# Kernel optimization log

Measured on AMD Instinct MI355X. Metric: run time of the kernel, lower is better.

Reference implementation:

```python
import jax, jax.numpy as jnp
import numpy as np

N_NODES = 50000
N_RAND_EDGES = 500000
SELF_LOOP_W = 0.5  # fill_value in add_remaining_self_loops


def _build_graph(key):
    k1, k2, k3 = jax.random.split(key, 3)
    src = jax.random.randint(k1, (N_RAND_EDGES,), 0, N_NODES)
    dst = jax.random.randint(k2, (N_RAND_EDGES,), 0, N_NODES)
    # PPMI weights are positive log-ratios; simulate with positive uniforms
    w = jax.random.uniform(k3, (N_RAND_EDGES,), minval=0.1, maxval=2.0)
    loops = jnp.arange(N_NODES)
    row = jnp.concatenate([src, loops])
    col = jnp.concatenate([dst, loops])
    ew = jnp.concatenate([w, jnp.full((N_NODES,), SELF_LOOP_W, dtype=w.dtype)])
    # symmetric normalization: D^-1/2 A D^-1/2 (deg computed from row, as in norm())
    deg = jax.ops.segment_sum(ew, row, num_segments=N_NODES)
    dis = jnp.where(deg > 0, deg ** -0.5, 0.0)
    norm = (dis[row] * ew * dis[col]).astype(jnp.float32)
    edge_index = jnp.stack([row, col]).astype(jnp.int64)
    return edge_index, norm


def setup_inputs() -> dict:
    key = jax.random.key(0)
    kx, kg, kw1, kw2 = jax.random.split(key, 4)
    edge_index, norm = _build_graph(kg)
    feat, hid, emb = 256, 128, 64
    # glorot init
    s1 = np.sqrt(6.0 / (feat + hid))
    s2 = np.sqrt(6.0 / (hid + emb))
    return {
        "x": jax.random.normal(kx, (N_NODES, feat), dtype=jnp.float32),
        "edge_index": edge_index,
        "norm": norm,
        "W1": jax.random.uniform(kw1, (feat, hid), minval=-s1, maxval=s1, dtype=jnp.float32),
        "b1": jnp.zeros((hid,), dtype=jnp.float32),
        "W2": jax.random.uniform(kw2, (hid, emb), minval=-s2, maxval=s2, dtype=jnp.float32),
        "b2": jnp.zeros((emb,), dtype=jnp.float32),
    }


def _gcn_layer(x, row, col, norm, W, b):
    h = x @ W                                   # [N, out]
    msg = norm[:, None] * h[row]                # gather + scale per edge
    agg = jax.ops.segment_sum(msg, col, num_segments=N_NODES)  # scatter-add
    return agg + b


def reference(x, edge_index, norm, W1, b1, W2, b2):
    row, col = edge_index[0], edge_index[1]
    h = _gcn_layer(x, row, col, norm, W1, b1)
    h = jax.nn.relu(h)  # dropout is identity in eval
    return _gcn_layer(h, row, col, norm, W2, b2)
```

## Files before the change

### kernel.cpp

```cpp
#include <hip/hip_runtime.h>
#include <stdint.h>


typedef __attribute__((ext_vector_type(8))) short short8;
typedef __attribute__((ext_vector_type(4))) float f32x4;

#define SLOTS 48
#define OCAP  65536

__device__ __forceinline__ unsigned short f2bf(float f) {
    unsigned u = __float_as_uint(f);
    return (unsigned short)((u + 0x7FFFu + ((u >> 16) & 1u)) >> 16);
}
__device__ __forceinline__ float bf_lo(unsigned v) { return __uint_as_float(v << 16); }
__device__ __forceinline__ float bf_hi(unsigned v) { return __uint_as_float(v & 0xFFFF0000u); }
__device__ __forceinline__ float bf1(unsigned short v) { return __uint_as_float((unsigned)v << 16); }
__device__ __forceinline__ unsigned short f2h(float f) {
    _Float16 h = (_Float16)f;
    return __builtin_bit_cast(unsigned short, h);
}
__device__ __forceinline__ float h2f(unsigned u16) {
    _Float16 h = __builtin_bit_cast(_Float16, (unsigned short)(u16 & 0xFFFFu));
    return (float)h;
}

__global__ __launch_bounds__(256) void k_prep(unsigned* __restrict__ ent, int entWords,
                                              int* __restrict__ cursor, int n,
                                              int* __restrict__ ocount,
                                              const int* __restrict__ ei,
                                              const float* __restrict__ nrm,
                                              int E, int N,
                                              unsigned* __restrict__ rec,
                                              const float* __restrict__ W1,
                                              const float* __restrict__ W2,
                                              unsigned short* __restrict__ W1t,
                                              unsigned short* __restrict__ W2t,
                                              int FEAT, int HID, int EMB) {
    __shared__ int sIs64;
    if (threadIdx.x < 64) {
        const int i = 1 + 2 * threadIdx.x;
        int z = (i < 2 * E) ? (ei[i] == 0) : 1;
        unsigned long long m = __ballot(z);
        if (threadIdx.x == 0) sIs64 = (m == ~0ULL) ? 1 : 0;
    }
    __syncthreads();
    const int is64 = sIs64;

    const int gid = blockIdx.x * blockDim.x + threadIdx.x;
    const int stride = gridDim.x * blockDim.x;
    if (gid == 0) *ocount = 0;

    int4* e4 = (int4*)ent;
    for (int j = gid; j < entWords / 4; j += stride) e4[j] = make_int4(0, 0, 0, 0);
    int4* c4 = (int4*)cursor;
    const int n4 = n >> 2;
    for (int j = gid; j < n4; j += stride) c4[j] = make_int4(0, 0, 0, 0);
    for (int j = (n4 << 2) + gid; j < n; j += stride) cursor[j] = 0;

    const int t1 = FEAT * HID, t2 = HID * EMB;
    for (int i = gid; i < t1 + t2; i += stride) {
        if (i < t1) {
            int k = i / HID, nn = i % HID;
            W1t[(size_t)nn * FEAT + k] = f2bf(W1[i]);
        } else {
            int j = i - t1;
            int k = j / EMB, nn = j % EMB;
            W2t[(size_t)nn * HID + k] = f2bf(W2[j]);
        }
    }

    const int nG = (E + 3) / 4;
    for (int g = gid; g < nG; g += stride) {
        const int e0 = g * 4;
        if (e0 + 3 < E) {
            int r[4], c[4];
            if (is64) {
                const int4* pr = (const int4*)(ei + 2 * e0);
                const int4* pc = (const int4*)(ei + 2 * E + 2 * e0);
                int4 r01 = pr[0], r23 = pr[1], c01 = pc[0], c23 = pc[1];
                r[0] = r01.x; r[1] = r01.z; r[2] = r23.x; r[3] = r23.z;
                c[0] = c01.x; c[1] = c01.z; c[2] = c23.x; c[3] = c23.z;
            } else {
                int4 rr = *(const int4*)(ei + e0);
                int4 cc = *(const int4*)(ei + E + e0);
                r[0] = rr.x; r[1] = rr.y; r[2] = rr.z; r[3] = rr.w;
                c[0] = cc.x; c[1] = cc.y; c[2] = cc.z; c[3] = cc.w;
            }
            const float4 w4 = *(const float4*)(nrm + e0);
            const float wv[4] = {w4.x, w4.y, w4.z, w4.w};
            unsigned ow[8];
            #pragma unroll
            for (int i = 0; i < 4; ++i) {
                unsigned a = 0xFFFFFFFFu, b = 0u;
                if ((unsigned)c[i] < (unsigned)N && (unsigned)r[i] < (unsigned)N) {
                    a = ((unsigned)r[i] << 16) | (unsigned)c[i];
                    b = (unsigned)f2h(wv[i]);
                }
                ow[2 * i + 0] = a;
                ow[2 * i + 1] = b;
            }
            uint4* dst = (uint4*)(rec + 2 * (size_t)e0);
            dst[0] = make_uint4(ow[0], ow[1], ow[2], ow[3]);
            dst[1] = make_uint4(ow[4], ow[5], ow[6], ow[7]);
        } else {
            for (int i = 0; i < 4; ++i) {
                const int e = e0 + i;
                unsigned a = 0xFFFFFFFFu, b = 0u;
                if (e < E) {
                    int rr, cc;
                    if (is64) { rr = ei[2 * e]; cc = ei[2 * (E + e)]; }
                    else      { rr = ei[e];     cc = ei[E + e]; }
                    if ((unsigned)cc < (unsigned)N && (unsigned)rr < (unsigned)N) {
                        a = ((unsigned)rr << 16) | (unsigned)cc;
                        b = (unsigned)f2h(nrm[e]);
                    }
                }
                rec[2 * (size_t)e + 0] = a;
                rec[2 * (size_t)e + 1] = b;
            }
        }
    }
}

template <int BM, int BN, int FM, int FN, bool A_F32, bool OUT_BF16>
__device__ __forceinline__ void gemm_body(char* ldsA, char* ldsB,
                                          const void* __restrict__ Ag,
                                          const unsigned short* __restrict__ Bt,
                                          void* __restrict__ Cv,
                                          int M, int K, int N, int blk) {
    const int tid  = threadIdx.x;
    const int lane = tid & 63;
    const int wid  = tid >> 6;
    const int wr   = wid >> 1;
    const int wc   = wid & 1;
    const int m0   = blk * BM;

    f32x4 acc[FM][FN] = {};

    for (int k0 = 0; k0 < K; k0 += 64) {
        {
            const int row  = tid >> 2;
            const int kq   = tid & 3;
            const int grow = min(m0 + row, M - 1);
            const int kbb  = kq * 32;
            const int sw   = (row & 7) << 4;
            if (A_F32) {
                const float* src = (const float*)Ag + (size_t)grow * K + k0 + kq * 16;
                float4 v0 = ((const float4*)src)[0];
                float4 v1 = ((const float4*)src)[1];
                float4 v2 = ((const float4*)src)[2];
                float4 v3 = ((const float4*)src)[3];
                union { short8 s; unsigned short h[8]; } p0, p1;
                p0.h[0] = f2bf(v0.x); p0.h[1] = f2bf(v0.y);
                p0.h[2] = f2bf(v0.z); p0.h[3] = f2bf(v0.w);
                p0.h[4] = f2bf(v1.x); p0.h[5] = f2bf(v1.y);
                p0.h[6] = f2bf(v1.z); p0.h[7] = f2bf(v1.w);
                p1.h[0] = f2bf(v2.x); p1.h[1] = f2bf(v2.y);
                p1.h[2] = f2bf(v2.z); p1.h[3] = f2bf(v2.w);
                p1.h[4] = f2bf(v3.x); p1.h[5] = f2bf(v3.y);
                p1.h[6] = f2bf(v3.z); p1.h[7] = f2bf(v3.w);
                *(short8*)(ldsA + row * 128 + ( kbb       ^ sw)) = p0.s;
                *(short8*)(ldsA + row * 128 + ((kbb + 16) ^ sw)) = p1.s;
            } else {
                const unsigned short* src =
                    (const unsigned short*)Ag + (size_t)grow * K + k0 + kq * 16;
                short8 s0 = ((const short8*)src)[0];
                short8 s1 = ((const short8*)src)[1];
                *(short8*)(ldsA + row * 128 + ( kbb       ^ sw)) = s0;
                *(short8*)(ldsA + row * 128 + ((kbb + 16) ^ sw)) = s1;
            }
        }
        if (BN == 128 || tid < 128) {
            const int row = tid >> 1;
            const int kh  = tid & 1;
            const int sw  = (row & 7) << 4;
            const short8* src = (const short8*)(Bt + (size_t)row * K + k0 + kh * 32);
            #pragma unroll
            for (int j = 0; j < 4; ++j) {
                short8 s = src[j];
                int kb = kh * 64 + j * 16;
                *(short8*)(ldsB + row * 128 + (kb ^ sw)) = s;
            }
        }
        __syncthreads();

        #pragma unroll
        for (int s = 0; s < 2; ++s) {
            const int klo = s * 64 + (lane >> 4) * 16;
            short8 af[FM], bfv[FN];
            #pragma unroll
            for (int i = 0; i < FM; ++i) {
                int r = wr * (FM * 16) + i * 16 + (lane & 15);
                af[i] = *(const short8*)(ldsA + r * 128 + (klo ^ ((r & 7) << 4)));
            }
            #pragma unroll
            for (int j = 0; j < FN; ++j) {
                int n = wc * (FN * 16) + j * 16 + (lane & 15);
                bfv[j] = *(const short8*)(ldsB + n * 128 + (klo ^ ((n & 7) << 4)));
            }
            #pragma unroll
            for (int i = 0; i < FM; ++i)
                #pragma unroll
                for (int j = 0; j < FN; ++j)
                    acc[i][j] = __builtin_amdgcn_mfma_f32_16x16x32_bf16(
                        af[i], bfv[j], acc[i][j], 0, 0, 0);
        }
        __syncthreads();
    }

    #pragma unroll
    for (int i = 0; i < FM; ++i) {
        const int rbase = m0 + wr * (FM * 16) + i * 16 + ((lane >> 4) << 2);
        #pragma unroll
        for (int j = 0; j < FN; ++j) {
            const int c = wc * (FN * 16) + j * 16 + (lane & 15);
            #pragma unroll
            for (int r = 0; r < 4; ++r)
                if (rbase + r < M) {
                    if (OUT_BF16)
                        ((unsigned short*)Cv)[(size_t)(rbase + r) * N + c] = f2bf(acc[i][j][r]);
                    else
                        ((float*)Cv)[(size_t)(rbase + r) * N + c] = acc[i][j][r];
                }
        }
    }
}

template <int BM, int BN, int FM, int FN, bool A_F32, bool OUT_BF16>
__global__ __launch_bounds__(256) void k_gemm_mfma(const void* __restrict__ Ag,
                                                   const unsigned short* __restrict__ Bt,
                                                   void* __restrict__ Cv,
                                                   int M, int K, int N) {
    __shared__ char ldsA[BM * 128];
    __shared__ char ldsB[BN * 128];
    gemm_body<BM, BN, FM, FN, A_F32, OUT_BF16>(ldsA, ldsB, Ag, Bt, Cv, M, K, N,
                                               blockIdx.x);
}

template <int BM, int BN, int FM, int FN, bool A_F32, bool OUT_BF16>
__global__ __launch_bounds__(256) void k_gemm_scatter(const void* __restrict__ Ag,
                                                      const unsigned short* __restrict__ Bt,
                                                      void* __restrict__ Cv,
                                                      int M, int K, int N,
                                                      int gemmBlocks,
                                                      const uint4* __restrict__ rec4,
                                                      int nPairs,
                                                      int* __restrict__ cursor,
                                                      unsigned* __restrict__ ent,
                                                      uint2* __restrict__ olist,
                                                      int* __restrict__ ocount) {
    __shared__ char ldsA[BM * 128];
    __shared__ char ldsB[BN * 128];
    if ((int)blockIdx.x < gemmBlocks) {
        gemm_body<BM, BN, FM, FN, A_F32, OUT_BF16>(ldsA, ldsB, Ag, Bt, Cv, M, K, N,
                                                   blockIdx.x);
    } else {
        const int t = (blockIdx.x - gemmBlocks) * blockDim.x + threadIdx.x;
        #pragma unroll
        for (int j = 0; j < 2; ++j) {
            const int p = 2 * t + j;
            if (p < nPairs) {
                const uint4 q = rec4[p];
                if (q.x != 0xFFFFFFFFu) {
                    const int d = (int)(q.x & 0xFFFFu);
                    const unsigned entry = (q.x & 0xFFFF0000u) | q.y;
                    const int pos = atomicAdd(&cursor[d], 1);
                    if (pos < SLOTS) ent[(size_t)d * SLOTS + pos] = entry;
                    else { int op = atomicAdd(ocount, 1);
                           if (op < OCAP) olist[op] = make_uint2((unsigned)d, entry); }
                }
                if (q.z != 0xFFFFFFFFu) {
                    const int d = (int)(q.z & 0xFFFFu);
                    const unsigned entry = (q.z & 0xFFFF0000u) | q.w;
                    const int pos = atomicAdd(&cursor[d], 1);
                    if (pos < SLOTS) ent[(size_t)d * SLOTS + pos] = entry;
                    else { int op = atomicAdd(ocount, 1);
                           if (op < OCAP) olist[op] = make_uint2((unsigned)d, entry); }
                }
            }
        }
    }
}

template <int F, bool RELU, bool OUT_BF16>
__global__ __launch_bounds__(256) void k_agg(const unsigned short* __restrict__ h,
                                             const unsigned* __restrict__ ent,
                                             const uint2* __restrict__ olist,
                                             const int* __restrict__ ocount,
                                             const float* __restrict__ bias,
                                             void* __restrict__ outp, int nnodes) {
    const int lane = threadIdx.x & 63;
    const int wid  = __builtin_amdgcn_readfirstlane(threadIdx.x >> 6);
    const int node = blockIdx.x * 4 + wid;
    if (node >= nnodes) return;
    const unsigned* slots = ent + (size_t)node * SLOTS;

    if (F == 128) {
        const unsigned* hp = (const unsigned*)h;
        float2 a0 = {0.f, 0.f}, a1 = {0.f, 0.f}, a2 = {0.f, 0.f}, a3 = {0.f, 0.f};
        uint4 q = *(const uint4*)(slots);
        for (int g = 0; g < SLOTS; g += 4) {
            if ((q.x | q.y | q.z | q.w) == 0u) break;
            const uint4 qn = *(const uint4*)(slots + g + 4);
            const float w0 = h2f(q.x), w1 = h2f(q.y), w2 = h2f(q.z), w3 = h2f(q.w);
            const unsigned v0 = hp[(size_t)(q.x >> 16) * 64 + lane];
            const unsigned v1 = hp[(size_t)(q.y >> 16) * 64 + lane];
            const unsigned v2 = hp[(size_t)(q.z >> 16) * 64 + lane];
            const unsigned v3 = hp[(size_t)(q.w >> 16) * 64 + lane];
            a0.x = fmaf(w0, bf_lo(v0), a0.x); a0.y = fmaf(w0, bf_hi(v0), a0.y);
            a1.x = fmaf(w1, bf_lo(v1), a1.x); a1.y = fmaf(w1, bf_hi(v1), a1.y);
            a2.x = fmaf(w2, bf_lo(v2), a2.x); a2.y = fmaf(w2, bf_hi(v2), a2.y);
            a3.x = fmaf(w3, bf_lo(v3), a3.x); a3.y = fmaf(w3, bf_hi(v3), a3.y);
            q = qn;
        }
        float2 acc;
        acc.x = (a0.x + a1.x) + (a2.x + a3.x);
        acc.y = (a0.y + a1.y) + (a2.y + a3.y);
        const int oc = *ocount;
        if (oc > 0) {
            for (int i = 0; i < oc && i < OCAP; ++i) {
                const uint2 it = olist[i];
                if ((int)it.x == node) {
                    const float w = h2f(it.y);
                    const unsigned v = hp[(size_t)(it.y >> 16) * 64 + lane];
                    acc.x = fmaf(w, bf_lo(v), acc.x);
                    acc.y = fmaf(w, bf_hi(v), acc.y);
                }
            }
        }
        const float2 b = ((const float2*)bias)[lane];
        acc.x += b.x; acc.y += b.y;
        if (RELU) { acc.x = fmaxf(acc.x, 0.f); acc.y = fmaxf(acc.y, 0.f); }
        if (OUT_BF16) {
            unsigned pack = (unsigned)f2bf(acc.x) | ((unsigned)f2bf(acc.y) << 16);
            ((unsigned*)outp)[(size_t)node * 64 + lane] = pack;
        } else {
            ((float2*)outp)[(size_t)node * 64 + lane] = acc;
        }
    } else {
        float a0 = 0.f, a1 = 0.f, a2 = 0.f, a3 = 0.f;
        uint4 q = *(const uint4*)(slots);
        for (int g = 0; g < SLOTS; g += 4) {
            if ((q.x | q.y | q.z | q.w) == 0u) break;
            const uint4 qn = *(const uint4*)(slots + g + 4);
            const float w0 = h2f(q.x), w1 = h2f(q.y), w2 = h2f(q.z), w3 = h2f(q.w);
            const float f0 = bf1(h[(size_t)(q.x >> 16) * 64 + lane]);
            const float f1 = bf1(h[(size_t)(q.y >> 16) * 64 + lane]);
            const float f2 = bf1(h[(size_t)(q.z >> 16) * 64 + lane]);
            const float f3 = bf1(h[(size_t)(q.w >> 16) * 64 + lane]);
            a0 = fmaf(w0, f0, a0); a1 = fmaf(w1, f1, a1);
            a2 = fmaf(w2, f2, a2); a3 = fmaf(w3, f3, a3);
            q = qn;
        }
        float acc = (a0 + a1) + (a2 + a3);
        const int oc = *ocount;
        if (oc > 0) {
            for (int i = 0; i < oc && i < OCAP; ++i) {
                const uint2 it = olist[i];
                if ((int)it.x == node)
                    acc = fmaf(h2f(it.y), bf1(h[(size_t)(it.y >> 16) * 64 + lane]), acc);
            }
        }
        acc += bias[lane];
        if (RELU) acc = fmaxf(acc, 0.f);
        ((float*)outp)[(size_t)node * 64 + lane] = acc;
    }
}


extern "C" void kernel_launch(void* const* d_in, const int* in_sizes, int n_in,
                              void* d_out, int out_size, void* d_ws, size_t ws_size,
                              hipStream_t stream) {
    const float* x   = (const float*)d_in[0];
    const int*   ei  = (const int*)d_in[1];
    const float* nrm = (const float*)d_in[2];
    const float* W1  = (const float*)d_in[3];
    const float* b1  = (const float*)d_in[4];
    const float* W2  = (const float*)d_in[5];
    const float* b2  = (const float*)d_in[6];
    float* out = (float*)d_out;

    const int HID  = in_sizes[4];
    const int FEAT = in_sizes[3] / HID;
    const int EMB  = in_sizes[5] / HID;
    const int Nn   = in_sizes[0] / FEAT;
    const int E    = in_sizes[2];
    const int E4   = (E + 3) & ~3;
    const int entWords = Nn * SLOTS;

    char* p = (char*)d_ws;
    auto alloc = [&](size_t bytes) {
        char* r = p;
        p += (bytes + 255) & ~(size_t)255;
        return r;
    };
    unsigned short* h1b    = (unsigned short*)alloc((size_t)Nn * HID * 2);
    unsigned short* a1b    = (unsigned short*)alloc((size_t)Nn * HID * 2);
    unsigned short* h2b    = (unsigned short*)alloc((size_t)Nn * EMB * 2);
    unsigned short* W1t    = (unsigned short*)alloc((size_t)HID * FEAT * 2);
    unsigned short* W2t    = (unsigned short*)alloc((size_t)EMB * HID * 2);
    int*            cursor = (int*)           alloc((size_t)Nn * 4);
    unsigned*       ent    = (unsigned*)      alloc((size_t)entWords * 4 + 256);
    unsigned*       rec    = (unsigned*)      alloc((size_t)E4 * 8);
    uint2*          olist  = (uint2*)         alloc((size_t)OCAP * 8);
    int*            ocount = (int*)           alloc(256);

    const int nPairs     = E4 / 2;
    const int sctBlocks  = (nPairs + 2 * 256 - 1) / (2 * 256);
    const int gemmBlocks = (Nn + 63) / 64;

    k_prep<<<1024, 256, 0, stream>>>(ent, entWords, cursor, Nn, ocount,
                                     ei, nrm, E, Nn, rec,
                                     W1, W2, W1t, W2t, FEAT, HID, EMB);
    k_gemm_scatter<64, 128, 2, 4, true, true>
        <<<gemmBlocks + sctBlocks, 256, 0, stream>>>(
            (const void*)x, W1t, (void*)h1b, Nn, FEAT, HID,
            gemmBlocks, (const uint4*)rec, nPairs, cursor, ent, olist, ocount);

    k_agg<128, true, true><<<(Nn + 3) / 4, 256, 0, stream>>>(
        h1b, ent, olist, ocount, b1, (void*)a1b, Nn);

    k_gemm_mfma<64, 64, 2, 2, false, true><<<gemmBlocks, 256, 0, stream>>>(
        (const void*)a1b, W2t, (void*)h2b, Nn, HID, EMB);
    k_agg<64, false, false><<<(Nn + 3) / 4, 256, 0, stream>>>(
        h2b, ent, olist, ocount, b2, (void*)out, Nn);
}
```

Baseline: 100.8 us.

## Fuse edge packing into scatter kernel and drop slot-table zeroing via cursor degrees

The intermediate packed-edge record buffer goes away. The scatter blocks of the fused GEMM+scatter kernel now read edge_index and norm directly and insert into the per-node slot table. The 50000×48-word slot table is no longer zeroed; the aggregation kernels read each node's degree from the cursor array and mask tail weights instead of stopping at zero sentinels. Row indices are clamped so garbage slots cannot read out of bounds. This removes a large memset and a write-then-read pass over the edge records, in exchange for an extra cursor load per node in aggregation.

Result: no change. 102.2 us (+1.4%).

```diff
diff --git a/kernel.cpp b/kernel.cpp
--- a/kernel.cpp
+++ b/kernel.cpp
@@ -24,39 +24,20 @@
     return (float)h;
 }
 
-__global__ __launch_bounds__(256) void k_prep(unsigned* __restrict__ ent, int entWords,
-                                              int* __restrict__ cursor, int n,
-                                              int* __restrict__ ocount,
-                                              const int* __restrict__ ei,
-                                              const float* __restrict__ nrm,
-                                              int E, int N,
-                                              unsigned* __restrict__ rec,
-                                              const float* __restrict__ W1,
-                                              const float* __restrict__ W2,
-                                              unsigned short* __restrict__ W1t,
-                                              unsigned short* __restrict__ W2t,
-                                              int FEAT, int HID, int EMB) {
-    __shared__ int sIs64;
-    if (threadIdx.x < 64) {
-        const int i = 1 + 2 * threadIdx.x;
-        int z = (i < 2 * E) ? (ei[i] == 0) : 1;
-        unsigned long long m = __ballot(z);
-        if (threadIdx.x == 0) sIs64 = (m == ~0ULL) ? 1 : 0;
-    }
-    __syncthreads();
-    const int is64 = sIs64;
-
+__global__ __launch_bounds__(256) void k_prep0(int* __restrict__ cursor, int n,
+                                               int* __restrict__ ocount,
+                                               const float* __restrict__ W1,
+                                               const float* __restrict__ W2,
+                                               unsigned short* __restrict__ W1t,
+                                               unsigned short* __restrict__ W2t,
+                                               int FEAT, int HID, int EMB) {
     const int gid = blockIdx.x * blockDim.x + threadIdx.x;
     const int stride = gridDim.x * blockDim.x;
     if (gid == 0) *ocount = 0;
-
-    int4* e4 = (int4*)ent;
-    for (int j = gid; j < entWords / 4; j += stride) e4[j] = make_int4(0, 0, 0, 0);
     int4* c4 = (int4*)cursor;
     const int n4 = n >> 2;
     for (int j = gid; j < n4; j += stride) c4[j] = make_int4(0, 0, 0, 0);
     for (int j = (n4 << 2) + gid; j < n; j += stride) cursor[j] = 0;
-
     const int t1 = FEAT * HID, t2 = HID * EMB;
     for (int i = gid; i < t1 + t2; i += stride) {
         if (i < t1) {
@@ -66,58 +47,6 @@
             int j = i - t1;
             int k = j / EMB, nn = j % EMB;
             W2t[(size_t)nn * HID + k] = f2bf(W2[j]);
-        }
-    }
-
-    const int nG = (E + 3) / 4;
-    for (int g = gid; g < nG; g += stride) {
-        const int e0 = g * 4;
-        if (e0 + 3 < E) {
-            int r[4], c[4];
-            if (is64) {
-                const int4* pr = (const int4*)(ei + 2 * e0);
-                const int4* pc = (const int4*)(ei + 2 * E + 2 * e0);
-                int4 r01 = pr[0], r23 = pr[1], c01 = pc[0], c23 = pc[1];
-                r[0] = r01.x; r[1] = r01.z; r[2] = r23.x; r[3] = r23.z;
-                c[0] = c01.x; c[1] = c01.z; c[2] = c23.x; c[3] = c23.z;
-            } else {
-                int4 rr = *(const int4*)(ei + e0);
-                int4 cc = *(const int4*)(ei + E + e0);
-                r[0] = rr.x; r[1] = rr.y; r[2] = rr.z; r[3] = rr.w;
-                c[0] = cc.x; c[1] = cc.y; c[2] = cc.z; c[3] = cc.w;
-            }
-            const float4 w4 = *(const float4*)(nrm + e0);
-            const float wv[4] = {w4.x, w4.y, w4.z, w4.w};
-            unsigned ow[8];
-            #pragma unroll
-            for (int i = 0; i < 4; ++i) {
-                unsigned a = 0xFFFFFFFFu, b = 0u;
-                if ((unsigned)c[i] < (unsigned)N && (unsigned)r[i] < (unsigned)N) {
-                    a = ((unsigned)r[i] << 16) | (unsigned)c[i];
-                    b = (unsigned)f2h(wv[i]);
-                }
-                ow[2 * i + 0] = a;
-                ow[2 * i + 1] = b;
-            }
-            uint4* dst = (uint4*)(rec + 2 * (size_t)e0);
-            dst[0] = make_uint4(ow[0], ow[1], ow[2], ow[3]);
-            dst[1] = make_uint4(ow[4], ow[5], ow[6], ow[7]);
-        } else {
-            for (int i = 0; i < 4; ++i) {
-                const int e = e0 + i;
-                unsigned a = 0xFFFFFFFFu, b = 0u;
-                if (e < E) {
-                    int rr, cc;
-                    if (is64) { rr = ei[2 * e]; cc = ei[2 * (E + e)]; }
-                    else      { rr = ei[e];     cc = ei[E + e]; }
-                    if ((unsigned)cc < (unsigned)N && (unsigned)rr < (unsigned)N) {
-                        a = ((unsigned)rr << 16) | (unsigned)cc;
-                        b = (unsigned)f2h(nrm[e]);
-                    }
-                }
-                rec[2 * (size_t)e + 0] = a;
-                rec[2 * (size_t)e + 1] = b;
-            }
         }
     }
 }
@@ -243,8 +172,9 @@
                                                       void* __restrict__ Cv,
                                                       int M, int K, int N,
                                                       int gemmBlocks,
-                                                      const uint4* __restrict__ rec4,
-                                                      int nPairs,
+                                                      const int* __restrict__ ei,
+                                                      const float* __restrict__ nrm,
+                                                      int E, int Nn,
                                                       int* __restrict__ cursor,
                                                       unsigned* __restrict__ ent,
                                                       uint2* __restrict__ olist,
@@ -254,36 +184,64 @@
     if ((int)blockIdx.x < gemmBlocks) {
         gemm_body<BM, BN, FM, FN, A_F32, OUT_BF16>(ldsA, ldsB, Ag, Bt, Cv, M, K, N,
                                                    blockIdx.x);
+        return;
+    }
+    __shared__ int sIs64;
+    if (threadIdx.x < 64) {
+        const int i = 1 + 2 * threadIdx.x;
+        int z = (i < 2 * E) ? (ei[i] == 0) : 1;
+        unsigned long long m = __ballot(z);
+        if (threadIdx.x == 0) sIs64 = (m == ~0ULL) ? 1 : 0;
+    }
+    __syncthreads();
+    const int is64 = sIs64;
+
+    const int t  = (blockIdx.x - gemmBlocks) * blockDim.x + threadIdx.x;
+    const int e0 = t * 4;
+    if (e0 >= E) return;
+
+    int r[4], c[4];
+    float wv[4];
+    int nv = 4;
+    if (e0 + 3 < E) {
+        if (is64) {
+            const int4* pr = (const int4*)(ei + 2 * e0);
+            const int4* pc = (const int4*)(ei + 2 * E + 2 * e0);
+            int4 r01 = pr[0], r23 = pr[1], c01 = pc[0], c23 = pc[1];
+            r[0] = r01.x; r[1] = r01.z; r[2] = r23.x; r[3] = r23.z;
+            c[0] = c01.x; c[1] = c01.z; c[2] = c23.x; c[3] = c23.z;
+        } else {
+            int4 rr = *(const int4*)(ei + e0);
+            int4 cc = *(const int4*)(ei + E + e0);
+            r[0] = rr.x; r[1] = rr.y; r[2] = rr.z; r[3] = rr.w;
+            c[0] = cc.x; c[1] = cc.y; c[2] = cc.z; c[3] = cc.w;
+        }
+        const float4 w4 = *(const float4*)(nrm + e0);
+        wv[0] = w4.x; wv[1] = w4.y; wv[2] = w4.z; wv[3] = w4.w;
     } else {
-        const int t = (blockIdx.x - gemmBlocks) * blockDim.x + threadIdx.x;
-        #pragma unroll
-        for (int j = 0; j < 2; ++j) {
-            const int p = 2 * t + j;
-            if (p < nPairs) {
-                const uint4 q = rec4[p];
-                if (q.x != 0xFFFFFFFFu) {
-                    const int d = (int)(q.x & 0xFFFFu);
-                    const unsigned entry = (q.x & 0xFFFF0000u) | q.y;
-                    const int pos = atomicAdd(&cursor[d], 1);
-                    if (pos < SLOTS) ent[(size_t)d * SLOTS + pos] = entry;
-                    else { int op = atomicAdd(ocount, 1);
-                           if (op < OCAP) olist[op] = make_uint2((unsigned)d, entry); }
-                }
-                if (q.z != 0xFFFFFFFFu) {
-                    const int d = (int)(q.z & 0xFFFFu);
-                    const unsigned entry = (q.z & 0xFFFF0000u) | q.w;
-                    const int pos = atomicAdd(&cursor[d], 1);
-                    if (pos < SLOTS) ent[(size_t)d * SLOTS + pos] = entry;
-                    else { int op = atomicAdd(ocount, 1);
-                           if (op < OCAP) olist[op] = make_uint2((unsigned)d, entry); }
-                }
-            }
+        nv = E - e0;
+        for (int i = 0; i < nv; ++i) {
+            const int e = e0 + i;
+            if (is64) { r[i] = ei[2 * e]; c[i] = ei[2 * (E + e)]; }
+            else      { r[i] = ei[e];     c[i] = ei[E + e]; }
+            wv[i] = nrm[e];
+        }
+    }
+    #pragma unroll
+    for (int i = 0; i < 4; ++i) {
+        if (i < nv && (unsigned)c[i] < (unsigned)Nn && (unsigned)r[i] < (unsigned)Nn) {
+            const unsigned entry = ((unsigned)r[i] << 16) | (unsigned)f2h(wv[i]);
+            const int pos = atomicAdd(&cursor[c[i]], 1);
+            if (pos < SLOTS) ent[(size_t)c[i] * SLOTS + pos] = entry;
+            else { int op = atomicAdd(ocount, 1);
+                   if (op < OCAP) olist[op] = make_uint2((unsigned)c[i], entry); }
         }
     }
 }
 
 template <int F, bool RELU, bool OUT_BF16>
 __global__ __launch_bounds__(256) void k_agg(const unsigned short* __restrict__ h,
+                                             const int* __restrict__ cursor,
                                              const unsigned* __restrict__ ent,
                                              const uint2* __restrict__ olist,
                                              const int* __restrict__ ocount,
@@ -293,25 +251,31 @@
     const int wid  = __builtin_amdgcn_readfirstlane(threadIdx.x >> 6);
     const int node = blockIdx.x * 4 + wid;
     if (node >= nnodes) return;
+    const int deg = min(cursor[node], SLOTS);
     const unsigned* slots = ent + (size_t)node * SLOTS;
+    const unsigned rmax = (unsigned)(nnodes - 1);
 
     if (F == 128) {
         const unsigned* hp = (const unsigned*)h;
         float2 a0 = {0.f, 0.f}, a1 = {0.f, 0.f}, a2 = {0.f, 0.f}, a3 = {0.f, 0.f};
-        uint4 q = *(const uint4*)(slots);
-        for (int g = 0; g < SLOTS; g += 4) {
-            if ((q.x | q.y | q.z | q.w) == 0u) break;
-            const uint4 qn = *(const uint4*)(slots + g + 4);
-            const float w0 = h2f(q.x), w1 = h2f(q.y), w2 = h2f(q.z), w3 = h2f(q.w);
-            const unsigned v0 = hp[(size_t)(q.x >> 16) * 64 + lane];
-            const unsigned v1 = hp[(size_t)(q.y >> 16) * 64 + lane];
-            const unsigned v2 = hp[(size_t)(q.z >> 16) * 64 + lane];
-            const unsigned v3 = hp[(size_t)(q.w >> 16) * 64 + lane];
+        for (int g = 0; g < deg; g += 4) {
+            uint4 q = *(const uint4*)(slots + g);
+            const int rem = deg - g;
+            float w0 = h2f(q.x), w1 = h2f(q.y), w2 = h2f(q.z), w3 = h2f(q.w);
+            if (rem < 4) {
+                w1 = (rem > 1) ? w1 : 0.f;
+                w2 = (rem > 2) ? w2 : 0.f;
+                w3 = 0.f;
+                if (rem == 3) w3 = 0.f; else if (rem > 3) {}
+            }
+            const unsigned v0 = hp[(size_t)min(q.x >> 16, rmax) * 64 + lane];
+            const unsigned v1 = hp[(size_t)min(q.y >> 16, rmax) * 64 + lane];
+            const unsigned v2 = hp[(size_t)min(q.z >> 16, rmax) * 64 + lane];
+            const unsigned v3 = hp[(size_t)min(q.w >> 16, rmax) * 64 + lane];
             a0.x = fmaf(w0, bf_lo(v0), a0.x); a0.y = fmaf(w0, bf_hi(v0), a0.y);
             a1.x = fmaf(w1, bf_lo(v1), a1.x); a1.y = fmaf(w1, bf_hi(v1), a1.y);
             a2.x = fmaf(w2, bf_lo(v2), a2.x); a2.y = fmaf(w2, bf_hi(v2), a2.y);
             a3.x = fmaf(w3, bf_lo(v3), a3.x); a3.y = fmaf(w3, bf_hi(v3), a3.y);
-            q = qn;
         }
         float2 acc;
         acc.x = (a0.x + a1.x) + (a2.x + a3.x);
@@ -322,7 +286,7 @@
                 const uint2 it = olist[i];
                 if ((int)it.x == node) {
                     const float w = h2f(it.y);
-                    const unsigned v = hp[(size_t)(it.y >> 16) * 64 + lane];
+                    const unsigned v = hp[(size_t)min(it.y >> 16, rmax) * 64 + lane];
                     acc.x = fmaf(w, bf_lo(v), acc.x);
                     acc.y = fmaf(w, bf_hi(v), acc.y);
                 }
@@ -339,18 +303,21 @@
         }
     } else {
         float a0 = 0.f, a1 = 0.f, a2 = 0.f, a3 = 0.f;
-        uint4 q = *(const uint4*)(slots);
-        for (int g = 0; g < SLOTS; g += 4) {
-            if ((q.x | q.y | q.z | q.w) == 0u) break;
-            const uint4 qn = *(const uint4*)(slots + g + 4);
-            const float w0 = h2f(q.x), w1 = h2f(q.y), w2 = h2f(q.z), w3 = h2f(q.w);
-            const float f0 = bf1(h[(size_t)(q.x >> 16) * 64 + lane]);
-            const float f1 = bf1(h[(size_t)(q.y >> 16) * 64 + lane]);
-            const float f2 = bf1(h[(size_t)(q.z >> 16) * 64 + lane]);
-            const float f3 = bf1(h[(size_t)(q.w >> 16) * 64 + lane]);
+        for (int g = 0; g < deg; g += 4) {
+            uint4 q = *(const uint4*)(slots + g);
+            const int rem = deg - g;
+            float w0 = h2f(q.x), w1 = h2f(q.y), w2 = h2f(q.z), w3 = h2f(q.w);
+            if (rem < 4) {
+                w1 = (rem > 1) ? w1 : 0.f;
+                w2 = (rem > 2) ? w2 : 0.f;
+                w3 = 0.f;
+            }
+            const float f0 = bf1(h[(size_t)min(q.x >> 16, rmax) * 64 + lane]);
+            const float f1 = bf1(h[(size_t)min(q.y >> 16, rmax) * 64 + lane]);
+            const float f2 = bf1(h[(size_t)min(q.z >> 16, rmax) * 64 + lane]);
+            const float f3 = bf1(h[(size_t)min(q.w >> 16, rmax) * 64 + lane]);
             a0 = fmaf(w0, f0, a0); a1 = fmaf(w1, f1, a1);
             a2 = fmaf(w2, f2, a2); a3 = fmaf(w3, f3, a3);
-            q = qn;
         }
         float acc = (a0 + a1) + (a2 + a3);
         const int oc = *ocount;
@@ -358,7 +325,8 @@
             for (int i = 0; i < oc && i < OCAP; ++i) {
                 const uint2 it = olist[i];
                 if ((int)it.x == node)
-                    acc = fmaf(h2f(it.y), bf1(h[(size_t)(it.y >> 16) * 64 + lane]), acc);
+                    acc = fmaf(h2f(it.y),
+                               bf1(h[(size_t)min(it.y >> 16, rmax) * 64 + lane]), acc);
             }
         }
         acc += bias[lane];
@@ -385,7 +353,6 @@
     const int EMB  = in_sizes[5] / HID;
     const int Nn   = in_sizes[0] / FEAT;
     const int E    = in_sizes[2];
-    const int E4   = (E + 3) & ~3;
     const int entWords = Nn * SLOTS;
 
     char* p = (char*)d_ws;
@@ -401,27 +368,24 @@
     unsigned short* W2t    = (unsigned short*)alloc((size_t)EMB * HID * 2);
     int*            cursor = (int*)           alloc((size_t)Nn * 4);
     unsigned*       ent    = (unsigned*)      alloc((size_t)entWords * 4 + 256);
-    unsigned*       rec    = (unsigned*)      alloc((size_t)E4 * 8);
     uint2*          olist  = (uint2*)         alloc((size_t)OCAP * 8);
     int*            ocount = (int*)           alloc(256);
 
-    const int nPairs     = E4 / 2;
-    const int sctBlocks  = (nPairs + 2 * 256 - 1) / (2 * 256);
+    const int sctBlocks  = (E + 4 * 256 - 1) / (4 * 256);
     const int gemmBlocks = (Nn + 63) / 64;
 
-    k_prep<<<1024, 256, 0, stream>>>(ent, entWords, cursor, Nn, ocount,
-                                     ei, nrm, E, Nn, rec,
+    k_prep0<<<128, 256, 0, stream>>>(cursor, Nn, ocount,
                                      W1, W2, W1t, W2t, FEAT, HID, EMB);
     k_gemm_scatter<64, 128, 2, 4, true, true>
         <<<gemmBlocks + sctBlocks, 256, 0, stream>>>(
             (const void*)x, W1t, (void*)h1b, Nn, FEAT, HID,
-            gemmBlocks, (const uint4*)rec, nPairs, cursor, ent, olist, ocount);
+            gemmBlocks, ei, nrm, E, Nn, cursor, ent, olist, ocount);
 
     k_agg<128, true, true><<<(Nn + 3) / 4, 256, 0, stream>>>(
-        h1b, ent, olist, ocount, b1, (void*)a1b, Nn);
+        h1b, cursor, ent, olist, ocount, b1, (void*)a1b, Nn);
 
     k_gemm_mfma<64, 64, 2, 2, false, true><<<gemmBlocks, 256, 0, stream>>>(
         (const void*)a1b, W2t, (void*)h2b, Nn, HID, EMB);
     k_agg<64, false, false><<<(Nn + 3) / 4, 256, 0, stream>>>(
-        h2b, ent, olist, ocount, b2, (void*)out, Nn);
-}
+        h2b, cursor, ent, olist, ocount, b2, (void*)out, Nn);
+}
```
